# Kernel optimization log

Hardware: AMD Instinct MI355X
Metric: run time of the kernel (lower is better)

## Reference

```python
import jax, jax.numpy as jnp
import numpy as np

H = 30          # num attention heads
KVH = 6         # num key/value heads
D = 64          # head dim
HID = 1920      # hidden size
THETA = 10000.0
WINDOW = 1024   # sliding window size
EPS = 1e-5


def setup_inputs() -> dict:
    key = jax.random.key(0)
    ks = jax.random.split(key, 8)
    B, S = 1, 2048
    scale = 0.02
    return {
        "hidden_states": jax.random.normal(ks[0], (B, S, HID), jnp.float32),
        "position_ids": jnp.arange(S, dtype=jnp.int64)[None, :],
        "Wq": jax.random.normal(ks[1], (H * D, HID), jnp.float32) * scale,
        "Wk": jax.random.normal(ks[2], (KVH * D, HID), jnp.float32) * scale,
        "Wv": jax.random.normal(ks[3], (KVH * D, HID), jnp.float32) * scale,
        "Wo": jax.random.normal(ks[4], (HID, H * D), jnp.float32) * scale,
        "q_ln_w": jnp.ones((H, D), jnp.float32) + 0.01 * jax.random.normal(ks[5], (H, D)),
        "k_ln_w": jnp.ones((KVH, D), jnp.float32) + 0.01 * jax.random.normal(ks[6], (KVH, D)),
        "q_alpha": jnp.ones((1,), jnp.float32),
        "k_alpha": jnp.ones((1,), jnp.float32),
        "v_alpha": jnp.ones((1,), jnp.float32),
        "o_alpha": jnp.ones((1,), jnp.float32),
    }


def _rotate_half(x):
    h = x.shape[-1] // 2
    return jnp.concatenate([-x[..., h:], x[..., :h]], axis=-1)


def _per_head_layernorm(x, w):
    # x: [B, nh, S, D]; w: [nh, D]; LayerNorm over D, no bias (biased variance as torch)
    mu = x.mean(-1, keepdims=True)
    var = jnp.mean((x - mu) ** 2, axis=-1, keepdims=True)
    return (x - mu) * jax.lax.rsqrt(var + EPS) * w[None, :, None, :]


def _rope_tables(seq_len):
    inv_freq = 1.0 / (THETA ** (jnp.arange(0, D, 2, dtype=jnp.float32) / D))
    t = jnp.arange(seq_len, dtype=jnp.float32)
    freqs = jnp.outer(t, inv_freq)                      # [S, D/2]
    emb = jnp.concatenate([freqs, freqs], axis=-1)      # [S, D]
    return jnp.cos(emb), jnp.sin(emb)


def reference(hidden_states, position_ids, Wq, Wk, Wv, Wo,
              q_ln_w, k_ln_w, q_alpha, k_alpha, v_alpha, o_alpha):
    B, S, _ = hidden_states.shape

    q = (hidden_states @ Wq.T) * q_alpha    # [B,S,H*D]
    k = (hidden_states @ Wk.T) * k_alpha    # [B,S,KVH*D]
    v = (hidden_states @ Wv.T) * v_alpha

    q = q.reshape(B, S, H, D).transpose(0, 2, 1, 3)      # [B,H,S,D]
    k = k.reshape(B, S, KVH, D).transpose(0, 2, 1, 3)    # [B,KVH,S,D]
    v = v.reshape(B, S, KVH, D).transpose(0, 2, 1, 3)

    # per-head LayerNorm on Q/K
    q = _per_head_layernorm(q, q_ln_w)
    k = _per_head_layernorm(k, k_ln_w)

    # RoPE in fp32, cos/sin gathered by position_ids and unsqueezed on head dim
    cos, sin = _rope_tables(S)                            # [S, D]
    cos = cos[position_ids][:, None, :, :]                # [B,1,S,D]
    sin = sin[position_ids][:, None, :, :]
    q = q.astype(jnp.float32) * cos + _rotate_half(q.astype(jnp.float32)) * sin
    k = k.astype(jnp.float32) * cos + _rotate_half(k.astype(jnp.float32)) * sin

    # GQA: repeat kv heads
    n_rep = H // KVH
    k = jnp.repeat(k, n_rep, axis=1)                      # [B,H,S,D]
    v = jnp.repeat(v, n_rep, axis=1)

    scores = jnp.einsum("bhqd,bhkd->bhqk", q, k) / jnp.sqrt(jnp.float32(D))

    # sliding-window causal mask: attend to j <= i and i - j < WINDOW
    i = jnp.arange(S)[:, None]
    j = jnp.arange(S)[None, :]
    mask = (j <= i) & ((i - j) < WINDOW)                  # [S,S]
    neg = jnp.finfo(jnp.float32).min
    scores = jnp.where(mask[None, None], scores, neg)

    attn = jax.nn.softmax(scores.astype(jnp.float32), axis=-1).astype(v.dtype)
    out = jnp.einsum("bhqk,bhkd->bhqd", attn, v)          # [B,H,S,D]
    out = out.transpose(0, 2, 1, 3).reshape(B, S, H * D)
    out = (out @ Wo.T) * o_alpha                          # [B,S,HID]
    return out
```

## Files before the change

kernel.cpp:

```cpp
#include <hip/hip_runtime.h>
#include <hip/hip_fp16.h>

#define SS 2048
#define HH 30
#define KVHH 6
#define DD 64
#define HIDD 1920
#define NQKV 2688

typedef __attribute__((ext_vector_type(4))) float  f32x4;
typedef __attribute__((ext_vector_type(4))) float  float4v;
typedef __attribute__((ext_vector_type(8))) _Float16 f16x8;
typedef __attribute__((ext_vector_type(4))) _Float16 f16x4;

__global__ __launch_bounds__(256) void rope_tab_init(float2* __restrict__ tab) {
    int idx = blockIdx.x * 256 + threadIdx.x;
    int s = idx >> 5, j = idx & 31;
    float f = exp2f(-13.287712379549449f * (float)j * (1.0f / 32.0f));
    float ang = (float)s * f;
    float sn, cs;
    sincosf(ang, &sn, &cs);
    tab[idx] = make_float2(cs, sn);
}

__global__ __launch_bounds__(256) void cvt_all(const float* __restrict__ hs,
                                               const float* __restrict__ Wq,
                                               const float* __restrict__ Wk,
                                               const float* __restrict__ Wv,
                                               const float* __restrict__ Wo,
                                               _Float16* __restrict__ hsb,
                                               _Float16* __restrict__ wqkvb,
                                               _Float16* __restrict__ wob,
                                               const float* __restrict__ qa,
                                               const float* __restrict__ ka,
                                               const float* __restrict__ va,
                                               const float* __restrict__ oa) {
    int b = blockIdx.x;
    const float* in; _Float16* out; float a; int base;
    if (b < 3840)      { in = hs; out = hsb;              a = 1.0f;  base = b; }
    else if (b < 7440) { in = Wq; out = wqkvb;            a = qa[0]; base = b - 3840; }
    else if (b < 8160) { in = Wk; out = wqkvb + 3686400;  a = ka[0]; base = b - 7440; }
    else if (b < 8880) { in = Wv; out = wqkvb + 4423680;  a = va[0]; base = b - 8160; }
    else               { in = Wo; out = wob;              a = oa[0]; base = b - 8880; }
    int i = base * 1024 + threadIdx.x * 4;
    float4v v = *(const float4v*)(in + i);
    f16x4 o;
    o[0] = (_Float16)(v[0] * a);
    o[1] = (_Float16)(v[1] * a);
    o[2] = (_Float16)(v[2] * a);
    o[3] = (_Float16)(v[3] * a);
    *(f16x4*)(out + i) = o;
}

#define GEMM_STAGE(buf, ktv)                                                                           \
    do {                                                                                               \
        _Pragma("unroll")                                                                              \
        for (int it = 0; it < 2; ++it) {                                                               \
            int gg  = it * 512 + tid;                                                                  \
            int row = gg >> 3;                                                                         \
            int sl  = (gg & 7) ^ (row & 7);                                                            \
            const _Float16* gA = A + (size_t)(m0 + row) * K + (ktv) + sl * 8;                          \
            const _Float16* gB = B + (size_t)(n0 + row) * K + (ktv) + sl * 8;                          \
            _Float16* lA = As[buf] + (size_t)(it * 512 + w * 64) * 8;                                  \
            _Float16* lB = Bs[buf] + (size_t)(it * 512 + w * 64) * 8;                                  \
            __builtin_amdgcn_global_load_lds((const __attribute__((address_space(1))) unsigned int*)gA,\
                                             (__attribute__((address_space(3))) unsigned int*)lA, 16, 0, 0); \
            __builtin_amdgcn_global_load_lds((const __attribute__((address_space(1))) unsigned int*)gB,\
                                             (__attribute__((address_space(3))) unsigned int*)lB, 16, 0, 0); \
        }                                                                                              \
    } while (0)

#define GEMM_BODY()                                                                                    \
    f32x4 acc[2][4];                                                                                   \
    _Pragma("unroll")                                                                                  \
    for (int a = 0; a < 2; ++a)                                                                        \
        _Pragma("unroll")                                                                              \
        for (int b = 0; b < 4; ++b) acc[a][b] = (f32x4)0.0f;                                           \
    GEMM_STAGE(0, 0);                                                                                  \
    const int nk = K >> 6;                                                                             \
    for (int t = 0; t < nk; ++t) {                                                                     \
        const int cur = t & 1;                                                                         \
        if (t + 1 < nk) {                                                                              \
            GEMM_STAGE(cur ^ 1, (t + 1) * 64);                                                         \
            asm volatile("s_waitcnt vmcnt(4)" ::: "memory");                                           \
        } else {                                                                                       \
            asm volatile("s_waitcnt vmcnt(0)" ::: "memory");                                           \
        }                                                                                              \
        __builtin_amdgcn_s_barrier();                                                                  \
        __builtin_amdgcn_sched_barrier(0);                                                             \
        _Pragma("unroll")                                                                              \
        for (int kk = 0; kk < 2; ++kk) {                                                               \
            f16x8 af[2], bf[4];                                                                        \
            _Pragma("unroll")                                                                          \
            for (int fm = 0; fm < 2; ++fm) {                                                           \
                int row = wm + fm * 16 + (l & 15);                                                     \
                int s   = (kk * 4 + (l >> 4)) ^ (row & 7);                                             \
                af[fm] = *(const f16x8*)(As[cur] + row * 64 + s * 8);                                  \
            }                                                                                          \
            _Pragma("unroll")                                                                          \
            for (int fn = 0; fn < 4; ++fn) {                                                           \
                int row = wn + fn * 16 + (l & 15);                                                     \
                int s   = (kk * 4 + (l >> 4)) ^ (row & 7);                                             \
                bf[fn] = *(const f16x8*)(Bs[cur] + row * 64 + s * 8);                                  \
            }                                                                                          \
            _Pragma("unroll")                                                                          \
            for (int fm = 0; fm < 2; ++fm)                                                             \
                _Pragma("unroll")                                                                      \
                for (int fn = 0; fn < 4; ++fn)                                                         \
                    acc[fm][fn] = __builtin_amdgcn_mfma_f32_16x16x32_f16(af[fm], bf[fn], acc[fm][fn], 0, 0, 0); \
        }                                                                                              \
        __builtin_amdgcn_sched_barrier(0);                                                             \
        __builtin_amdgcn_s_barrier();                                                                  \
    }

__global__ __launch_bounds__(512) void gemm_qkv(const _Float16* __restrict__ A,
                                                const _Float16* __restrict__ B,
                                                const float* __restrict__ qlnw,
                                                const float* __restrict__ klnw,
                                                const float2* __restrict__ tab,
                                                _Float16* __restrict__ Qh,
                                                _Float16* __restrict__ Kh,
                                                _Float16* __restrict__ Vh,
                                                int M, int N, int K) {
    __shared__ __align__(16) _Float16 As[2][128 * 64];
    __shared__ __align__(16) _Float16 Bs[2][128 * 64];
    const int tid = threadIdx.x;
    const int l   = tid & 63;
    const int w   = tid >> 6;
    const int wm  = (w >> 1) * 32;
    const int wn  = (w & 1) * 64;
    const int g = l >> 4, li = l & 15;

    const int gx  = gridDim.x;
    const int nwg = gx * gridDim.y;
    int bid = blockIdx.y * gx + blockIdx.x;
    int lid = (bid & 7) * (nwg >> 3) + (bid >> 3);
    int gsz = gx * 8;
    int grp = lid / gsz;
    int r   = lid - grp * gsz;
    int bx  = r >> 3;
    int by  = grp * 8 + (r & 7);

    const int m0 = by * 128;
    const int n0 = bx * 128;

    GEMM_BODY();

    const int unit = (n0 >> 6) + (w & 1);
    if (unit < 36) {
        const float* lwp = (unit < 30) ? (qlnw + unit * 64) : (klnw + (unit - 30) * 64);
        float lw[4];
#pragma unroll
        for (int fn = 0; fn < 4; ++fn) lw[fn] = lwp[fn * 16 + li];
        _Float16* outp = (unit < 30) ? (Qh + (size_t)unit * SS * 64)
                                     : (Kh + (size_t)(unit - 30) * SS * 64);
        const float qs = (unit < 30) ? 0.18033688011112042f : 1.0f;
#pragma unroll
        for (int fm = 0; fm < 2; ++fm)
#pragma unroll
            for (int j = 0; j < 4; ++j) {
                float x0 = acc[fm][0][j], x1 = acc[fm][1][j], x2 = acc[fm][2][j], x3 = acc[fm][3][j];
                float s1 = x0 + x1 + x2 + x3;
                float s2 = x0 * x0 + x1 * x1 + x2 * x2 + x3 * x3;
#pragma unroll
                for (int off = 1; off < 16; off <<= 1) {
                    s1 += __shfl_xor(s1, off);
                    s2 += __shfl_xor(s2, off);
                }
                float mu  = s1 * (1.0f / 64.0f);
                float var = s2 * (1.0f / 64.0f) - mu * mu;
                float rst = rsqrtf(var + 1e-5f);
                float n0_ = (x0 - mu) * rst * lw[0];
                float n1_ = (x1 - mu) * rst * lw[1];
                float n2_ = (x2 - mu) * rst * lw[2];
                float n3_ = (x3 - mu) * rst * lw[3];
                int srow = m0 + wm + fm * 16 + g * 4 + j;
                float2 cs0 = tab[srow * 32 + li];
                float2 cs1 = tab[srow * 32 + 16 + li];
                float o0 = (n0_ * cs0.x - n2_ * cs0.y) * qs;
                float o1 = (n1_ * cs1.x - n3_ * cs1.y) * qs;
                float o2 = (n2_ * cs0.x + n0_ * cs0.y) * qs;
                float o3 = (n3_ * cs1.x + n1_ * cs1.y) * qs;
                _Float16* rp = outp + (size_t)srow * 64 + li;
                rp[0]  = (_Float16)o0;
                rp[16] = (_Float16)o1;
                rp[32] = (_Float16)o2;
                rp[48] = (_Float16)o3;
            }
    } else {
        _Float16* outp = Vh + (size_t)(unit - 36) * SS * 64;
#pragma unroll
        for (int fm = 0; fm < 2; ++fm)
#pragma unroll
            for (int j = 0; j < 4; ++j) {
                int srow = m0 + wm + fm * 16 + g * 4 + j;
                _Float16* rp = outp + (size_t)srow * 64 + li;
                rp[0]  = (_Float16)acc[fm][0][j];
                rp[16] = (_Float16)acc[fm][1][j];
                rp[32] = (_Float16)acc[fm][2][j];
                rp[48] = (_Float16)acc[fm][3][j];
            }
    }
}

__global__ __launch_bounds__(512) void gemm_bt_f16(const _Float16* __restrict__ A,
                                                   const _Float16* __restrict__ B,
                                                   float* __restrict__ C,
                                                   int M, int N, int K) {
    __shared__ __align__(16) _Float16 As[2][128 * 64];
    __shared__ __align__(16) _Float16 Bs[2][128 * 64];
    const int tid = threadIdx.x;
    const int l   = tid & 63;
    const int w   = tid >> 6;
    const int wm  = (w >> 1) * 32;
    const int wn  = (w & 1) * 64;

    const int gx  = gridDim.x;
    const int nwg = gx * gridDim.y;
    int bid = blockIdx.y * gx + blockIdx.x;
    int lid = (bid & 7) * (nwg >> 3) + (bid >> 3);
    int gsz = gx * 8;
    int grp = lid / gsz;
    int r   = lid - grp * gsz;
    int bx  = r >> 3;
    int by  = grp * 8 + (r & 7);

    const int m0 = by * 128;
    const int n0 = bx * 128;

    GEMM_BODY();

#pragma unroll
    for (int fm = 0; fm < 2; ++fm)
#pragma unroll
        for (int fn = 0; fn < 4; ++fn)
#pragma unroll
            for (int j = 0; j < 4; ++j) {
                int rr = m0 + wm + fm * 16 + (l >> 4) * 4 + j;
                int cc = n0 + wn + fn * 16 + (l & 15);
                C[(size_t)rr * N + cc] = acc[fm][fn][j];
            }
}

__global__ __launch_bounds__(256) void transpose_v(const _Float16* __restrict__ Vh,
                                                   _Float16* __restrict__ Vt) {
    __shared__ _Float16 T[64][68];
    const int s0 = blockIdx.x * 64;
    const int h  = blockIdx.y;
    const int tid = threadIdx.x;
#pragma unroll
    for (int pass = 0; pass < 2; ++pass) {
        int idx = pass * 256 + tid;
        int r = idx >> 3, d0 = (idx & 7) * 8;
        f16x8 v = *(const f16x8*)(Vh + ((size_t)(h * SS + s0 + r)) * 64 + d0);
#pragma unroll
        for (int j = 0; j < 8; ++j) T[r][d0 + j] = v[j];
    }
    __syncthreads();
#pragma unroll
    for (int pass = 0; pass < 2; ++pass) {
        int idx = pass * 256 + tid;
        int d = idx >> 3, c0 = (idx & 7) * 8;
        f16x8 o;
#pragma unroll
        for (int j = 0; j < 8; ++j) o[j] = T[c0 + j][d];
        *(f16x8*)(Vt + ((size_t)(h * 64 + d)) * SS + s0 + c0) = o;
    }
}

#define ATTN_STAGE(buf, c)                                                                             \
    do {                                                                                               \
        _Pragma("unroll")                                                                              \
        for (int t = 0; t < 2; ++t) {                                                                  \
            int rloc = w * 16 + t * 8 + (l >> 3);                                                      \
            int ss = (l & 7) ^ (l >> 3);                                                               \
            const _Float16* gK = Kh + ((size_t)kvh * SS + (c) * 64 + rloc) * 64 + ss * 8;              \
            const _Float16* gV = Vt + ((size_t)kvh * 64 + rloc) * SS + (c) * 64 + ss * 8;              \
            _Float16* lK = Ks[buf] + (w * 16 + t * 8) * 64;                                            \
            _Float16* lV = Vs[buf] + (w * 16 + t * 8) * 64;                                            \
            __builtin_amdgcn_global_load_lds((const __attribute__((address_space(1))) unsigned int*)gK,\
                                             (__attribute__((address_space(3))) unsigned int*)lK, 16, 0, 0); \
            __builtin_amdgcn_global_load_lds((const __attribute__((address_space(1))) unsigned int*)gV,\
                                             (__attribute__((address_space(3))) unsigned int*)lV, 16, 0, 0); \
        }                                                                                              \
    } while (0)

__global__ __launch_bounds__(256) void attn_mfma(const _Float16* __restrict__ Qh,
                                                 const _Float16* __restrict__ Kh,
                                                 const _Float16* __restrict__ Vt,
                                                 _Float16* __restrict__ Ob) {
    __shared__ __align__(16) _Float16 Ks[2][64 * 64];
    __shared__ __align__(16) _Float16 Vs[2][64 * 64];
    __shared__ __align__(16) _Float16 Ps[4][16 * 64];

    const int qb = 31 - blockIdx.y;
    const int h = blockIdx.x;
    const int Q0 = qb * 64;
    const int kvh = h / 5;
    const int tid = threadIdx.x, l = tid & 63, w = tid >> 6;
    const int g = l >> 4, li = l & 15;
    const int qabs = Q0 + w * 16 + li;
    const int qw = Q0 + w * 16;

    f16x8 qf[2];
#pragma unroll
    for (int dk = 0; dk < 2; ++dk)
        qf[dk] = *(const f16x8*)(Qh + ((size_t)h * SS + qabs) * 64 + dk * 32 + g * 8);
    asm volatile("s_waitcnt vmcnt(0)" ::: "memory");

    float m_i = -1e20f, l_i = 0.0f;
    f32x4 o[4];
#pragma unroll
    for (int fn = 0; fn < 4; ++fn) o[fn] = (f32x4)0.0f;

    const int c_lo = (Q0 >= 1023) ? ((Q0 - 1023) >> 6) : 0;
    const int c_hi = qb;

    ATTN_STAGE(0, c_lo);

    for (int c = c_lo; c <= c_hi; ++c) {
        const int nb = (c - c_lo) & 1;
        if (c < c_hi) {
            ATTN_STAGE(nb ^ 1, c + 1);
            asm volatile("s_waitcnt vmcnt(4)" ::: "memory");
        } else {
            asm volatile("s_waitcnt vmcnt(0)" ::: "memory");
        }
        __builtin_amdgcn_s_barrier();
        __builtin_amdgcn_sched_barrier(0);

        if (c * 64 <= qw + 15 && c * 64 + 63 >= qw - 1023) {
            const _Float16* Kb = Ks[nb];
            const _Float16* Vb = Vs[nb];
            const bool full = (c * 64 + 63 <= qw) && (c * 64 >= qw + 15 - 1023);

            f32x4 st[4];
#pragma unroll
            for (int f = 0; f < 4; ++f) st[f] = (f32x4)0.0f;
            __builtin_amdgcn_s_setprio(1);
#pragma unroll
            for (int dk = 0; dk < 2; ++dk) {
#pragma unroll
                for (int f = 0; f < 4; ++f) {
                    int ps = (dk * 4 + g) ^ (li & 7);
                    f16x8 kf = *(const f16x8*)(Kb + (f * 16 + li) * 64 + ps * 8);
                    st[f] = __builtin_amdgcn_mfma_f32_16x16x32_f16(kf, qf[dk], st[f], 0, 0, 0);
                }
            }
            __builtin_amdgcn_s_setprio(0);

            if (!full) {
#pragma unroll
                for (int f = 0; f < 4; ++f)
#pragma unroll
                    for (int reg = 0; reg < 4; ++reg) {
                        int kab = c * 64 + f * 16 + g * 4 + reg;
                        bool valid = (kab <= qabs) && (qabs - kab < 1024);
                        st[f][reg] = valid ? st[f][reg] : -1e30f;
                    }
            }
            float mx = -1e30f;
#pragma unroll
            for (int f = 0; f < 4; ++f)
#pragma unroll
                for (int reg = 0; reg < 4; ++reg) mx = fmaxf(mx, st[f][reg]);
            mx = fmaxf(mx, __shfl_xor(mx, 16));
            mx = fmaxf(mx, __shfl_xor(mx, 32));

            if (__any(mx > m_i + 8.0f)) {
                float m_new = fmaxf(m_i, mx);
                float corr = exp2f(m_i - m_new);
                m_i = m_new;
                l_i *= corr;
                float c0 = __shfl(corr, g * 4 + 0);
                float c1 = __shfl(corr, g * 4 + 1);
                float c2 = __shfl(corr, g * 4 + 2);
                float c3 = __shfl(corr, g * 4 + 3);
#pragma unroll
                for (int fn = 0; fn < 4; ++fn) {
                    o[fn][0] *= c0; o[fn][1] *= c1; o[fn][2] *= c2; o[fn][3] *= c3;
                }
            }

            float psum = 0.0f;
            char* Pw = (char*)&Ps[w][0] + li * 128;
#pragma unroll
            for (int f = 0; f < 4; ++f)
#pragma unroll
                for (int rp = 0; rp < 2; ++rp) {
                    float p0 = exp2f(st[f][2 * rp]     - m_i);
                    float p1 = exp2f(st[f][2 * rp + 1] - m_i);
                    psum += p0 + p1;
                    union { _Float16 hh[2]; unsigned u; } pk;
                    pk.hh[0] = (_Float16)p0; pk.hh[1] = (_Float16)p1;
                    int phys = (f * 2 + (g >> 1)) ^ (li & 7);
                    *(unsigned*)(Pw + phys * 16 + (g & 1) * 8 + rp * 4) = pk.u;
                }
            psum += __shfl_xor(psum, 16);
            psum += __shfl_xor(psum, 32);
            l_i += psum;

            __builtin_amdgcn_s_setprio(1);
#pragma unroll
            for (int kk = 0; kk < 2; ++kk) {
                int pp = (kk * 4 + g) ^ (li & 7);
                f16x8 pa = *(const f16x8*)(Pw + pp * 16);
#pragma unroll
                for (int fn = 0; fn < 4; ++fn) {
                    int drow = fn * 16 + li;
                    int vp = (kk * 4 + g) ^ (li & 7);
                    f16x8 vf = *(const f16x8*)(Vb + drow * 64 + vp * 8);
                    o[fn] = __builtin_amdgcn_mfma_f32_16x16x32_f16(pa, vf, o[fn], 0, 0, 0);
                }
            }
            __builtin_amdgcn_s_setprio(0);
        }
        __builtin_amdgcn_sched_barrier(0);
        __builtin_amdgcn_s_barrier();
    }

#pragma unroll
    for (int reg = 0; reg < 4; ++reg) {
        float linv = 1.0f / __shfl(l_i, g * 4 + reg);
        int row = Q0 + w * 16 + g * 4 + reg;
#pragma unroll
        for (int fn = 0; fn < 4; ++fn)
            Ob[(size_t)row * HIDD + h * 64 + fn * 16 + li] = (_Float16)(o[fn][reg] * linv);
    }
}

extern "C" void kernel_launch(void* const* d_in, const int* in_sizes, int n_in,
                              void* d_out, int out_size, void* d_ws, size_t ws_size,
                              hipStream_t stream) {
    const float* hs   = (const float*)d_in[0];
    const float* Wq   = (const float*)d_in[2];
    const float* Wk   = (const float*)d_in[3];
    const float* Wv   = (const float*)d_in[4];
    const float* Wo   = (const float*)d_in[5];
    const float* qlnw = (const float*)d_in[6];
    const float* klnw = (const float*)d_in[7];
    const float* qa   = (const float*)d_in[8];
    const float* ka   = (const float*)d_in[9];
    const float* va   = (const float*)d_in[10];
    const float* oa   = (const float*)d_in[11];

    char* ws = (char*)d_ws;
    _Float16* hsb   = (_Float16*)ws;                 ws += (size_t)SS * HIDD * 2;
    _Float16* wqkvb = (_Float16*)ws;                 ws += (size_t)NQKV * HIDD * 2;
    _Float16* wob   = (_Float16*)ws;                 ws += (size_t)HIDD * HIDD * 2;
    float2*   rtab  = (float2*)ws;                   ws += (size_t)SS * 32 * 8;
    _Float16* Qhd   = (_Float16*)ws;                 ws += (size_t)HH * SS * DD * 2;
    _Float16* Khd   = (_Float16*)ws;                 ws += (size_t)KVHH * SS * DD * 2;
    _Float16* Vhd   = (_Float16*)ws;                 ws += (size_t)KVHH * SS * DD * 2;
    _Float16* Vtd   = (_Float16*)ws;                 ws += (size_t)KVHH * SS * DD * 2;
    _Float16* attnb = (_Float16*)ws;                 ws += (size_t)SS * HIDD * 2;

    rope_tab_init<<<256, 256, 0, stream>>>(rtab);

    cvt_all<<<12480, 256, 0, stream>>>(hs, Wq, Wk, Wv, Wo, hsb, wqkvb, wob, qa, ka, va, oa);

    gemm_qkv<<<dim3(NQKV / 128, SS / 128), 512, 0, stream>>>(hsb, wqkvb, qlnw, klnw, rtab,
                                                             Qhd, Khd, Vhd, SS, NQKV, HIDD);

    transpose_v<<<dim3(SS / 64, KVHH), 256, 0, stream>>>(Vhd, Vtd);

    attn_mfma<<<dim3(HH, SS / 64), 256, 0, stream>>>(Qhd, Khd, Vtd, attnb);

    gemm_bt_f16<<<dim3(HIDD / 128, SS / 128), 512, 0, stream>>>(attnb, wob, (float*)d_out, SS, HIDD, HIDD);
}
```

Measured before the change: 126.4 us.

## Process two KV chunks per barrier with a four-slot LDS prefetch ring

The attention loop now stages K/V tiles in pairs into a four-slot LDS ring and handles two 64-key chunks between each pair of barriers. This halves the barrier and waitcnt points and prefetches further ahead. The cost is double the K/V LDS footprint, which can lower the number of resident blocks per CU. When the chunk count is odd, the prefetch reads one chunk past the valid range. The fp16 packing of P also switches to a single pkrtz conversion, which truncates instead of rounding to nearest.

```diff
diff --git a/kernel.cpp b/kernel.cpp
--- a/kernel.cpp
+++ b/kernel.cpp
@@ -268,7 +268,7 @@
     }
 }
 
-#define ATTN_STAGE(buf, c)                                                                             \
+#define ATTN_STAGE(slot, c)                                                                            \
     do {                                                                                               \
         _Pragma("unroll")                                                                              \
         for (int t = 0; t < 2; ++t) {                                                                  \
@@ -276,8 +276,8 @@
             int ss = (l & 7) ^ (l >> 3);                                                               \
             const _Float16* gK = Kh + ((size_t)kvh * SS + (c) * 64 + rloc) * 64 + ss * 8;              \
             const _Float16* gV = Vt + ((size_t)kvh * 64 + rloc) * SS + (c) * 64 + ss * 8;              \
-            _Float16* lK = Ks[buf] + (w * 16 + t * 8) * 64;                                            \
-            _Float16* lV = Vs[buf] + (w * 16 + t * 8) * 64;                                            \
+            _Float16* lK = KsB + (slot) * 4096 + (w * 16 + t * 8) * 64;                                \
+            _Float16* lV = VsB + (slot) * 4096 + (w * 16 + t * 8) * 64;                                \
             __builtin_amdgcn_global_load_lds((const __attribute__((address_space(1))) unsigned int*)gK,\
                                              (__attribute__((address_space(3))) unsigned int*)lK, 16, 0, 0); \
             __builtin_amdgcn_global_load_lds((const __attribute__((address_space(1))) unsigned int*)gV,\
@@ -289,8 +289,8 @@
                                                  const _Float16* __restrict__ Kh,
                                                  const _Float16* __restrict__ Vt,
                                                  _Float16* __restrict__ Ob) {
-    __shared__ __align__(16) _Float16 Ks[2][64 * 64];
-    __shared__ __align__(16) _Float16 Vs[2][64 * 64];
+    __shared__ __align__(16) _Float16 KsB[4 * 4096];
+    __shared__ __align__(16) _Float16 VsB[4 * 4096];
     __shared__ __align__(16) _Float16 Ps[4][16 * 64];
 
     const int qb = 31 - blockIdx.y;
@@ -317,103 +317,109 @@
     const int c_hi = qb;
 
     ATTN_STAGE(0, c_lo);
-
-    for (int c = c_lo; c <= c_hi; ++c) {
-        const int nb = (c - c_lo) & 1;
-        if (c < c_hi) {
-            ATTN_STAGE(nb ^ 1, c + 1);
-            asm volatile("s_waitcnt vmcnt(4)" ::: "memory");
+    ATTN_STAGE(1, c_lo + 1);
+
+    int pair = 0;
+    for (int c = c_lo; c <= c_hi; c += 2, pair ^= 1) {
+        const int sb = pair * 2;
+        if (c + 2 <= c_hi) {
+            ATTN_STAGE(sb ^ 2, c + 2);
+            ATTN_STAGE((sb ^ 2) + 1, c + 3);
+            asm volatile("s_waitcnt vmcnt(8)" ::: "memory");
         } else {
             asm volatile("s_waitcnt vmcnt(0)" ::: "memory");
         }
         __builtin_amdgcn_s_barrier();
         __builtin_amdgcn_sched_barrier(0);
 
-        if (c * 64 <= qw + 15 && c * 64 + 63 >= qw - 1023) {
-            const _Float16* Kb = Ks[nb];
-            const _Float16* Vb = Vs[nb];
-            const bool full = (c * 64 + 63 <= qw) && (c * 64 >= qw + 15 - 1023);
-
-            f32x4 st[4];
-#pragma unroll
-            for (int f = 0; f < 4; ++f) st[f] = (f32x4)0.0f;
-            __builtin_amdgcn_s_setprio(1);
-#pragma unroll
-            for (int dk = 0; dk < 2; ++dk) {
-#pragma unroll
-                for (int f = 0; f < 4; ++f) {
-                    int ps = (dk * 4 + g) ^ (li & 7);
-                    f16x8 kf = *(const f16x8*)(Kb + (f * 16 + li) * 64 + ps * 8);
-                    st[f] = __builtin_amdgcn_mfma_f32_16x16x32_f16(kf, qf[dk], st[f], 0, 0, 0);
+#pragma unroll
+        for (int sc = 0; sc < 2; ++sc) {
+            const int cc = c + sc;
+            if (cc * 64 <= qw + 15 && cc * 64 + 63 >= qw - 1023) {
+                const _Float16* Kb = KsB + (sb + sc) * 4096;
+                const _Float16* Vb = VsB + (sb + sc) * 4096;
+                const bool full = (cc * 64 + 63 <= qw) && (cc * 64 >= qw + 15 - 1023);
+
+                f32x4 st[4];
+#pragma unroll
+                for (int f = 0; f < 4; ++f) st[f] = (f32x4)0.0f;
+                __builtin_amdgcn_s_setprio(1);
+#pragma unroll
+                for (int dk = 0; dk < 2; ++dk) {
+#pragma unroll
+                    for (int f = 0; f < 4; ++f) {
+                        int ps = (dk * 4 + g) ^ (li & 7);
+                        f16x8 kf = *(const f16x8*)(Kb + (f * 16 + li) * 64 + ps * 8);
+                        st[f] = __builtin_amdgcn_mfma_f32_16x16x32_f16(kf, qf[dk], st[f], 0, 0, 0);
+                    }
                 }
+                __builtin_amdgcn_s_setprio(0);
+
+                if (!full) {
+#pragma unroll
+                    for (int f = 0; f < 4; ++f)
+#pragma unroll
+                        for (int reg = 0; reg < 4; ++reg) {
+                            int kab = cc * 64 + f * 16 + g * 4 + reg;
+                            bool valid = (kab <= qabs) && (qabs - kab < 1024);
+                            st[f][reg] = valid ? st[f][reg] : -1e30f;
+                        }
+                }
+                float mx = -1e30f;
+#pragma unroll
+                for (int f = 0; f < 4; ++f)
+#pragma unroll
+                    for (int reg = 0; reg < 4; ++reg) mx = fmaxf(mx, st[f][reg]);
+                mx = fmaxf(mx, __shfl_xor(mx, 16));
+                mx = fmaxf(mx, __shfl_xor(mx, 32));
+
+                if (__any(mx > m_i + 8.0f)) {
+                    float m_new = fmaxf(m_i, mx);
+                    float corr = exp2f(m_i - m_new);
+                    m_i = m_new;
+                    l_i *= corr;
+                    float c0 = __shfl(corr, g * 4 + 0);
+                    float c1 = __shfl(corr, g * 4 + 1);
+                    float c2 = __shfl(corr, g * 4 + 2);
+                    float c3 = __shfl(corr, g * 4 + 3);
+#pragma unroll
+                    for (int fn = 0; fn < 4; ++fn) {
+                        o[fn][0] *= c0; o[fn][1] *= c1; o[fn][2] *= c2; o[fn][3] *= c3;
+                    }
+                }
+
+                float psum = 0.0f;
+                char* Pw = (char*)&Ps[w][0] + li * 128;
+#pragma unroll
+                for (int f = 0; f < 4; ++f)
+#pragma unroll
+                    for (int rp = 0; rp < 2; ++rp) {
+                        float p0 = exp2f(st[f][2 * rp]     - m_i);
+                        float p1 = exp2f(st[f][2 * rp + 1] - m_i);
+                        psum += p0 + p1;
+                        auto pk = __builtin_amdgcn_cvt_pkrtz(p0, p1);
+                        int phys = (f * 2 + (g >> 1)) ^ (li & 7);
+                        *(decltype(pk)*)(Pw + phys * 16 + (g & 1) * 8 + rp * 4) = pk;
+                    }
+                psum += __shfl_xor(psum, 16);
+                psum += __shfl_xor(psum, 32);
+                l_i += psum;
+
+                __builtin_amdgcn_s_setprio(1);
+#pragma unroll
+                for (int kk = 0; kk < 2; ++kk) {
+                    int pp = (kk * 4 + g) ^ (li & 7);
+                    f16x8 pa = *(const f16x8*)(Pw + pp * 16);
+#pragma unroll
+                    for (int fn = 0; fn < 4; ++fn) {
+                        int drow = fn * 16 + li;
+                        int vp = (kk * 4 + g) ^ (li & 7);
+                        f16x8 vf = *(const f16x8*)(Vb + drow * 64 + vp * 8);
+                        o[fn] = __builtin_amdgcn_mfma_f32_16x16x32_f16(pa, vf, o[fn], 0, 0, 0);
+                    }
+                }
+                __builtin_amdgcn_s_setprio(0);
             }
-            __builtin_amdgcn_s_setprio(0);
-
-            if (!full) {
-#pragma unroll
-                for (int f = 0; f < 4; ++f)
-#pragma unroll
-                    for (int reg = 0; reg < 4; ++reg) {
-                        int kab = c * 64 + f * 16 + g * 4 + reg;
-                        bool valid = (kab <= qabs) && (qabs - kab < 1024);
-                        st[f][reg] = valid ? st[f][reg] : -1e30f;
-                    }
-            }
-            float mx = -1e30f;
-#pragma unroll
-            for (int f = 0; f < 4; ++f)
-#pragma unroll
-                for (int reg = 0; reg < 4; ++reg) mx = fmaxf(mx, st[f][reg]);
-            mx = fmaxf(mx, __shfl_xor(mx, 16));
-            mx = fmaxf(mx, __shfl_xor(mx, 32));
-
-            if (__any(mx > m_i + 8.0f)) {
-                float m_new = fmaxf(m_i, mx);
-                float corr = exp2f(m_i - m_new);
-                m_i = m_new;
-                l_i *= corr;
-                float c0 = __shfl(corr, g * 4 + 0);
-                float c1 = __shfl(corr, g * 4 + 1);
-                float c2 = __shfl(corr, g * 4 + 2);
-                float c3 = __shfl(corr, g * 4 + 3);
-#pragma unroll
-                for (int fn = 0; fn < 4; ++fn) {
-                    o[fn][0] *= c0; o[fn][1] *= c1; o[fn][2] *= c2; o[fn][3] *= c3;
-                }
-            }
-
-            float psum = 0.0f;
-            char* Pw = (char*)&Ps[w][0] + li * 128;
-#pragma unroll
-            for (int f = 0; f < 4; ++f)
-#pragma unroll
-                for (int rp = 0; rp < 2; ++rp) {
-                    float p0 = exp2f(st[f][2 * rp]     - m_i);
-                    float p1 = exp2f(st[f][2 * rp + 1] - m_i);
-                    psum += p0 + p1;
-                    union { _Float16 hh[2]; unsigned u; } pk;
-                    pk.hh[0] = (_Float16)p0; pk.hh[1] = (_Float16)p1;
-                    int phys = (f * 2 + (g >> 1)) ^ (li & 7);
-                    *(unsigned*)(Pw + phys * 16 + (g & 1) * 8 + rp * 4) = pk.u;
-                }
-            psum += __shfl_xor(psum, 16);
-            psum += __shfl_xor(psum, 32);
-            l_i += psum;
-
-            __builtin_amdgcn_s_setprio(1);
-#pragma unroll
-            for (int kk = 0; kk < 2; ++kk) {
-                int pp = (kk * 4 + g) ^ (li & 7);
-                f16x8 pa = *(const f16x8*)(Pw + pp * 16);
-#pragma unroll
-                for (int fn = 0; fn < 4; ++fn) {
-                    int drow = fn * 16 + li;
-                    int vp = (kk * 4 + g) ^ (li & 7);
-                    f16x8 vf = *(const f16x8*)(Vb + drow * 64 + vp * 8);
-                    o[fn] = __builtin_amdgcn_mfma_f32_16x16x32_f16(pa, vf, o[fn], 0, 0, 0);
-                }
-            }
-            __builtin_amdgcn_s_setprio(0);
         }
         __builtin_amdgcn_sched_barrier(0);
         __builtin_amdgcn_s_barrier();
```

After: 134.1 us. +6.2%, slower.
